# Kernel tuning notes

Hardware: AMD Instinct MI355X
Metric: run time of the kernel (lower is better)

Reference implementation:

```python
import jax, jax.numpy as jnp
import numpy as np

N_NODES = 500000


def _gconv(x, src, dst, ew, w_neigh, b, w_self):
    # DGL GraphConv(norm='none'): multiply weight first (in>=out here), then aggregate.
    h = x @ w_neigh                      # [N, out]
    msg = h[src] * ew[:, None]           # [E, out]
    agg = jax.ops.segment_sum(msg, dst, num_segments=N_NODES)
    return agg + b + x @ w_self          # neigh conv (+bias) + self-loop linear (no bias)


def setup_inputs() -> dict:
    key = jax.random.key(0)
    ks = jax.random.split(key, 16)
    N, E, G, F = N_NODES, 16000000, 64, 16
    inp = {
        "x": jax.random.normal(ks[0], (N, F), jnp.float32),
        "src": jax.random.randint(ks[1], (E,), 0, N),
        "dst": jax.random.randint(ks[2], (E,), 0, N),
        "graph_id": jnp.sort(jax.random.randint(ks[3], (N,), 0, G)),
        "edge_weight": jax.random.uniform(ks[4], (E,), jnp.float32),
        "num_graphs": G,
        "w_neigh0": jax.random.normal(ks[5], (F, 1), jnp.float32),
        "b0": jax.random.normal(ks[6], (1,), jnp.float32),
        "w_self0": jax.random.normal(ks[7], (F, 1), jnp.float32),
        "w_neigh1": jax.random.normal(ks[8], (1, 1), jnp.float32),
        "b1": jax.random.normal(ks[9], (1,), jnp.float32),
        "w_self1": jax.random.normal(ks[10], (1, 1), jnp.float32),
        "w_neigh2": jax.random.normal(ks[11], (1, 1), jnp.float32),
        "b2": jax.random.normal(ks[12], (1,), jnp.float32),
        "w_self2": jax.random.normal(ks[13], (1, 1), jnp.float32),
        "fc1_w": jax.random.normal(ks[14], (8, 1), jnp.float32),
        "fc1_b": jax.random.normal(ks[15], (8,), jnp.float32),
        "out_w": jax.random.normal(jax.random.fold_in(key, 100), (4, 8), jnp.float32),
        "out_b": jax.random.normal(jax.random.fold_in(key, 101), (4,), jnp.float32),
    }
    return inp


def reference(x, src, dst, graph_id, edge_weight, num_graphs,
              w_neigh0, b0, w_self0, w_neigh1, b1, w_self1,
              w_neigh2, b2, w_self2, fc1_w, fc1_b, out_w, out_b):
    h = jax.nn.relu(_gconv(x, src, dst, edge_weight, w_neigh0, b0, w_self0))
    h = jax.nn.relu(_gconv(h, src, dst, edge_weight, w_neigh1, b1, w_self1))
    h = jax.nn.relu(_gconv(h, src, dst, edge_weight, w_neigh2, b2, w_self2))
    # dgl.sum_nodes: per-graph segment sum over batched graph -> [G, 1]
    hg = jax.ops.segment_sum(h, graph_id, num_segments=num_graphs)
    hg2 = jax.nn.sigmoid((hg @ fc1_w.T + fc1_b) * 1000.0)   # [G, 8]
    out = jax.nn.relu(hg2 @ out_w.T + out_b)                # [G, 4]
    return jax.nn.log_softmax(out, axis=1)
```

## Files before the change

### kernel.cpp

```cpp
#include <hip/hip_runtime.h>
#include <hip/hip_fp16.h>

#define N_NODES 500000
#define NGRAPH  64
#define FDIM    16
#define NB1     62
#define NPB1    8192
#define SH1     13
#define SLC     16
#define NBLK    1024
#define CH      4096
typedef unsigned int u32;
typedef unsigned short u16;
typedef unsigned long long u64;

__global__ __launch_bounds__(1024) void proj_hist(const int* __restrict__ dst, int E, int chunk,
                                                  u32* __restrict__ blockHist,
                                                  const float* __restrict__ x,
                                                  const float* __restrict__ wn,
                                                  const float* __restrict__ wsf,
                                                  float* __restrict__ a,
                                                  float* __restrict__ s) {
    __shared__ u32 cnt[NB1];
    if (blockIdx.x < NBLK) {
        if (threadIdx.x < NB1) cnt[threadIdx.x] = 0;
        __syncthreads();
        int b = blockIdx.x;
        int lo = b * chunk, hi = min(lo + chunk, E);
        int m = (hi - lo) & ~3;
        for (int i = lo + threadIdx.x * 4; i < lo + m; i += 4096) {
            int4 d = *(const int4*)(dst + i);
            atomicAdd(&cnt[((u32)d.x) >> SH1], 1u);
            atomicAdd(&cnt[((u32)d.y) >> SH1], 1u);
            atomicAdd(&cnt[((u32)d.z) >> SH1], 1u);
            atomicAdd(&cnt[((u32)d.w) >> SH1], 1u);
        }
        for (int i = lo + m + threadIdx.x; i < hi; i += 1024)
            atomicAdd(&cnt[((u32)dst[i]) >> SH1], 1u);
        __syncthreads();
        if (threadIdx.x < NB1)
            blockHist[(size_t)b * NB1 + threadIdx.x] = cnt[threadIdx.x];
    } else {
        int i = (blockIdx.x - NBLK) * 1024 + threadIdx.x;
        if (i >= N_NODES) return;
        const float4* xr = (const float4*)(x + (size_t)i * FDIM);
        float4 v0 = xr[0], v1 = xr[1], v2 = xr[2], v3 = xr[3];
        const float4* n4 = (const float4*)wn;
        const float4* s4 = (const float4*)wsf;
        float4 n0 = n4[0], n1 = n4[1], n2 = n4[2], n3 = n4[3];
        float4 w0 = s4[0], w1 = s4[1], w2 = s4[2], w3 = s4[3];
        float an = v0.x*n0.x + v0.y*n0.y + v0.z*n0.z + v0.w*n0.w
                 + v1.x*n1.x + v1.y*n1.y + v1.z*n1.z + v1.w*n1.w
                 + v2.x*n2.x + v2.y*n2.y + v2.z*n2.z + v2.w*n2.w
                 + v3.x*n3.x + v3.y*n3.y + v3.z*n3.z + v3.w*n3.w;
        float as = v0.x*w0.x + v0.y*w0.y + v0.z*w0.z + v0.w*w0.w
                 + v1.x*w1.x + v1.y*w1.y + v1.z*w1.z + v1.w*w1.w
                 + v2.x*w2.x + v2.y*w2.y + v2.z*w2.z + v2.w*w2.w
                 + v3.x*w3.x + v3.y*w3.y + v3.z*w3.z + v3.w*w3.w;
        a[i] = an;
        s[i] = as;
    }
}

__global__ __launch_bounds__(NBLK) void scan1_kernel(u32* __restrict__ blockHist,
                                                     u32* __restrict__ binTotal) {
    int j = blockIdx.x;
    __shared__ u32 lsum[NBLK];
    int t = threadIdx.x;
    u32 v = blockHist[(size_t)t * NB1 + j];
    lsum[t] = v;
    __syncthreads();
    u32 x = v;
    for (int off = 1; off < NBLK; off <<= 1) {
        u32 y = (t >= off) ? lsum[t - off] : 0u;
        __syncthreads();
        x += y; lsum[t] = x;
        __syncthreads();
    }
    if (t == NBLK - 1) binTotal[j] = x;
    blockHist[(size_t)t * NB1 + j] = x - v;
}

__global__ void scan2_kernel(const u32* __restrict__ binTotal, u32* __restrict__ binStart) {
    __shared__ u32 sh[64];
    int t = threadIdx.x;
    u32 v = (t < NB1) ? binTotal[t] : 0u;
    sh[t] = v;
    __syncthreads();
    for (int d = 1; d < 64; d <<= 1) {
        u32 y = (t >= d) ? sh[t - d] : 0u;
        __syncthreads();
        sh[t] += y;
        __syncthreads();
    }
    if (t < NB1) binStart[t] = sh[t] - v;
    if (t == 63) binStart[NB1] = sh[63];
}

__global__ __launch_bounds__(512) void scatter_staged(const int* __restrict__ src,
                                                      const int* __restrict__ dst,
                                                      const float* __restrict__ ew,
                                                      int E, int chunk,
                                                      const u32* __restrict__ blockHist,
                                                      const u32* __restrict__ binStart,
                                                      u32* __restrict__ bIdx,
                                                      u16* __restrict__ bW) {
    __shared__ u32 cursor[64];
    __shared__ u32 cnt[64];
    __shared__ u32 off[64];
    __shared__ u64 stage[CH];
    __shared__ unsigned char binOf[CH];
    int b = blockIdx.x, tid = threadIdx.x;
    if (tid < NB1) cursor[tid] = binStart[tid] + blockHist[(size_t)b * NB1 + tid];
    int lo = b * chunk, hiB = min(lo + chunk, E);
    for (int base = lo; base < hiB; base += CH) {
        int n = min(CH, hiB - base);
        if (tid < 64) cnt[tid] = 0;
        __syncthreads();
        u32 rec[8]; u16 wv[8]; u32 bi[8], rk[8];
#pragma unroll
        for (int k = 0; k < 8; ++k) {
            int idx = base + k * 512 + tid;
            bi[k] = 0xFFFFFFFFu;
            if (idx < base + n) {
                u32 d  = (u32)dst[idx];
                bi[k]  = d >> SH1;
                rec[k] = ((u32)src[idx]) | ((d & (NPB1 - 1)) << 19);
                wv[k]  = __half_as_ushort(__float2half(ew[idx]));
                rk[k]  = atomicAdd(&cnt[bi[k]], 1u);
            }
        }
        __syncthreads();
        if (tid < 64) off[tid] = cnt[tid];
        __syncthreads();
        for (int d2 = 1; d2 < 64; d2 <<= 1) {
            u32 y = 0;
            if (tid < 64 && tid >= d2) y = off[tid - d2];
            __syncthreads();
            if (tid < 64) off[tid] += y;
            __syncthreads();
        }
        if (tid < 64) off[tid] -= cnt[tid];
        __syncthreads();
#pragma unroll
        for (int k = 0; k < 8; ++k) {
            if (bi[k] != 0xFFFFFFFFu) {
                u32 p = off[bi[k]] + rk[k];
                stage[p] = (u64)rec[k] | ((u64)wv[k] << 32);
                binOf[p] = (unsigned char)bi[k];
            }
        }
        __syncthreads();
        for (int p = tid; p < n; p += 512) {
            u32 jj = binOf[p];
            u64 e = stage[p];
            u32 gpos = cursor[jj] + ((u32)p - off[jj]);
            bIdx[gpos] = (u32)e;
            bW[gpos]   = (u16)(e >> 32);
        }
        __syncthreads();
        if (tid < NB1) cursor[tid] += cnt[tid];
        __syncthreads();
    }
}

__global__ __launch_bounds__(512) void bin_pass(const u32* __restrict__ bIdx,
                                                const u16* __restrict__ bW,
                                                const u32* __restrict__ binStart,
                                                const float* __restrict__ hsrc,
                                                float* __restrict__ partials) {
    __shared__ float acc[NPB1];
    int j = blockIdx.x / SLC, sl = blockIdx.x % SLC;
    for (int t = threadIdx.x; t < NPB1; t += 512) acc[t] = 0.0f;
    __syncthreads();
    u32 blo = binStart[j], bhi = binStart[j + 1];
    u32 cj = bhi - blo;
    u32 per = (cj + SLC - 1) / SLC;
    u32 lo = blo + sl * per;
    u32 hi = min(lo + per, bhi);
    u32 i = lo + threadIdx.x;
    for (; i + 7u * 512u < hi; i += 8u * 512u) {
        u32 r[8]; u16 w[8];
#pragma unroll
        for (int k = 0; k < 8; ++k) r[k] = __builtin_nontemporal_load(&bIdx[i + (u32)k * 512u]);
#pragma unroll
        for (int k = 0; k < 8; ++k) w[k] = __builtin_nontemporal_load(&bW[i + (u32)k * 512u]);
        float g[8];
#pragma unroll
        for (int k = 0; k < 8; ++k) g[k] = hsrc[r[k] & 0x7FFFFu];
#pragma unroll
        for (int k = 0; k < 8; ++k)
            atomicAdd(&acc[r[k] >> 19], g[k] * __half2float(__ushort_as_half(w[k])));
    }
    for (; i < hi; i += 512) {
        u32 r = __builtin_nontemporal_load(&bIdx[i]);
        u16 w = __builtin_nontemporal_load(&bW[i]);
        atomicAdd(&acc[r >> 19], hsrc[r & 0x7FFFFu] * __half2float(__ushort_as_half(w)));
    }
    __syncthreads();
    float* p = partials + ((size_t)j * SLC + sl) * NPB1;
    for (int t = threadIdx.x; t < NPB1; t += 512)
        __builtin_nontemporal_store(acc[t], &p[t]);
}

template<bool LAST>
__global__ __launch_bounds__(256) void merge_update(const float* __restrict__ partials,
                                                    const float* __restrict__ selfv,
                                                    const float* __restrict__ wnp,
                                                    const float* __restrict__ bp,
                                                    const float* __restrict__ wsp,
                                                    float* __restrict__ hout,
                                                    const int* __restrict__ gid,
                                                    float* __restrict__ hg) {
    int n = blockIdx.x * blockDim.x + threadIdx.x;
    if (n >= N_NODES) return;
    int j = n >> SH1;
    int l = n & (NPB1 - 1);
    const float* p = partials + ((size_t)j * SLC) * NPB1 + l;
    float sum = 0.0f;
#pragma unroll
    for (int k = 0; k < SLC; ++k) sum += __builtin_nontemporal_load(&p[k * NPB1]);
    float scale = wnp ? wnp[0] : 1.0f;
    float wself = wsp ? wsp[0] : 1.0f;
    float v = fmaxf(sum * scale + bp[0] + selfv[n] * wself, 0.0f);
    hout[n] = v;
    if (LAST) {
        int g = gid[n];
        unsigned long long act = __ballot(1);
        int g0 = __shfl(g, 0);
        if (act == ~0ull && __all(g == g0)) {
            float t = v;
#pragma unroll
            for (int o = 32; o > 0; o >>= 1) t += __shfl_down(t, o);
            if ((threadIdx.x & 63) == 0) atomicAdd(&hg[g0], t);
        } else {
            atomicAdd(&hg[g], v);
        }
    }
}

__global__ void edge_pass(const int* __restrict__ src, const int* __restrict__ dst,
                          const float* __restrict__ ew, const float* __restrict__ h,
                          float* __restrict__ agg, const float* __restrict__ wnp, int E) {
    float scale = wnp ? wnp[0] : 1.0f;
    int stride = gridDim.x * blockDim.x;
    for (int i = blockIdx.x * blockDim.x + threadIdx.x; i < E; i += stride)
        atomicAdd(&agg[dst[i]], h[src[i]] * ew[i] * scale);
}
__global__ void node_update(const float* __restrict__ agg, const float* __restrict__ selfv,
                            const float* __restrict__ bp, const float* __restrict__ wsp,
                            float* __restrict__ hout) {
    int i = blockIdx.x * blockDim.x + threadIdx.x;
    if (i >= N_NODES) return;
    float wsc = wsp ? wsp[0] : 1.0f;
    hout[i] = fmaxf(agg[i] + bp[0] + selfv[i] * wsc, 0.0f);
}
__global__ void proj_kernel(const float* __restrict__ x, const float* __restrict__ wn,
                            const float* __restrict__ wsf, float* __restrict__ a,
                            float* __restrict__ s) {
    int i = blockIdx.x * blockDim.x + threadIdx.x;
    if (i >= N_NODES) return;
    float an = 0.f, as = 0.f;
    for (int k = 0; k < FDIM; ++k) {
        float v = x[(size_t)i * FDIM + k];
        an += v * wn[k]; as += v * wsf[k];
    }
    a[i] = an; s[i] = as;
}

__global__ __launch_bounds__(256) void graph_sum(const float* __restrict__ h,
                                                 const int* __restrict__ gid,
                                                 float* __restrict__ hg) {
    __shared__ float loc[NGRAPH];
    int t = threadIdx.x;
    if (t < NGRAPH) loc[t] = 0.0f;
    __syncthreads();
    int nq = N_NODES / 4;
    int stride = gridDim.x * blockDim.x;
    for (int q = blockIdx.x * blockDim.x + t; q < nq; q += stride) {
        int4   g4 = *(const int4*)(gid + 4 * q);
        float4 h4 = *(const float4*)(h + 4 * q);
        int g0 = __shfl(g4.x, 0);
        bool uni = (g4.x == g0) & (g4.w == g0);
        if (__all(uni)) {
            float v = h4.x + h4.y + h4.z + h4.w;
#pragma unroll
            for (int o = 32; o > 0; o >>= 1) v += __shfl_down(v, o);
            if ((t & 63) == 0) atomicAdd(&loc[g0], v);
        } else {
            atomicAdd(&loc[g4.x], h4.x);
            atomicAdd(&loc[g4.y], h4.y);
            atomicAdd(&loc[g4.z], h4.z);
            atomicAdd(&loc[g4.w], h4.w);
        }
    }
    __syncthreads();
    if (t < NGRAPH) atomicAdd(&hg[t], loc[t]);
}

__global__ void head_kernel(const float* __restrict__ hg,
                            const float* __restrict__ fc1w, const float* __restrict__ fc1b,
                            const float* __restrict__ outw, const float* __restrict__ outb,
                            float* __restrict__ out) {
    int g = threadIdx.x;
    if (g >= NGRAPH) return;
    float v = hg[g];
    float t[8];
#pragma unroll
    for (int j = 0; j < 8; ++j) {
        float z = (v * fc1w[j] + fc1b[j]) * 1000.0f;
        t[j] = 1.0f / (1.0f + expf(-z));
    }
    float o[4];
#pragma unroll
    for (int k = 0; k < 4; ++k) {
        float acc2 = outb[k];
#pragma unroll
        for (int j = 0; j < 8; ++j) acc2 += t[j] * outw[k * 8 + j];
        o[k] = fmaxf(acc2, 0.0f);
    }
    float m = fmaxf(fmaxf(o[0], o[1]), fmaxf(o[2], o[3]));
    float se = 0.0f;
#pragma unroll
    for (int k = 0; k < 4; ++k) se += expf(o[k] - m);
    float lse = m + logf(se);
#pragma unroll
    for (int k = 0; k < 4; ++k) out[g * 4 + k] = o[k] - lse;
}

extern "C" void kernel_launch(void* const* d_in, const int* in_sizes, int n_in,
                              void* d_out, int out_size, void* d_ws, size_t ws_size,
                              hipStream_t stream) {
    const float* x    = (const float*)d_in[0];
    const int*   src  = (const int*)  d_in[1];
    const int*   dst  = (const int*)  d_in[2];
    const int*   gid  = (const int*)  d_in[3];
    const float* ew   = (const float*)d_in[4];
    const float* wn0  = (const float*)d_in[6];
    const float* b0   = (const float*)d_in[7];
    const float* ws0  = (const float*)d_in[8];
    const float* wn1  = (const float*)d_in[9];
    const float* b1   = (const float*)d_in[10];
    const float* ws1  = (const float*)d_in[11];
    const float* wn2  = (const float*)d_in[12];
    const float* b2   = (const float*)d_in[13];
    const float* ws2  = (const float*)d_in[14];
    const float* fc1w = (const float*)d_in[15];
    const float* fc1b = (const float*)d_in[16];
    const float* outw = (const float*)d_in[17];
    const float* outb = (const float*)d_in[18];
    int E = in_sizes[1];

    const int BLK = 256;
    int nodeGrid = (N_NODES + BLK - 1) / BLK;
    char* ws = (char*)d_ws;

    size_t off = 0;
    u32* bIdx       = (u32*)(ws + off); off += (size_t)E * 4;
    u16* bW         = (u16*)(ws + off); off += (size_t)E * 2;
    off = (off + 63) & ~(size_t)63;
    u32* blockHist  = (u32*)(ws + off); off += (size_t)NBLK * NB1 * 4;
    u32* binStart   = (u32*)(ws + off); off += (NB1 + 2) * 4;
    off = (off + 63) & ~(size_t)63;
    u32* binTotal   = (u32*)(ws + off); off += (NB1 + 2) * 4;
    off = (off + 63) & ~(size_t)63;
    float* partials = (float*)(ws + off); off += (size_t)NB1 * SLC * NPB1 * 4;
    float* a  = (float*)(ws + off); off += (size_t)N_NODES * 4;
    float* s  = (float*)(ws + off); off += (size_t)N_NODES * 4;
    float* hg = (float*)(ws + off); off += 256;
    size_t need = off;

    if (ws_size >= need) {
        int chunk = (((E + NBLK - 1) / NBLK) + 3) & ~3;
        int projBlocks = (N_NODES + 1023) / 1024;

        proj_hist<<<NBLK + projBlocks, 1024, 0, stream>>>(dst, E, chunk, blockHist,
                                                          x, wn0, ws0, a, s);
        scan1_kernel<<<NB1, NBLK, 0, stream>>>(blockHist, binTotal);
        scan2_kernel<<<1, 64, 0, stream>>>(binTotal, binStart);
        scatter_staged<<<NBLK, 512, 0, stream>>>(src, dst, ew, E, chunk, blockHist,
                                                 binStart, bIdx, bW);
        (void)hipMemsetAsync(hg, 0, NGRAPH * sizeof(float), stream);

        bin_pass<<<NB1 * SLC, 512, 0, stream>>>(bIdx, bW, binStart, a, partials);
        merge_update<false><<<nodeGrid, BLK, 0, stream>>>(partials, s, nullptr, b0, nullptr,
                                                          s, gid, hg);
        bin_pass<<<NB1 * SLC, 512, 0, stream>>>(bIdx, bW, binStart, s, partials);
        merge_update<false><<<nodeGrid, BLK, 0, stream>>>(partials, s, wn1, b1, ws1,
                                                          s, gid, hg);
        bin_pass<<<NB1 * SLC, 512, 0, stream>>>(bIdx, bW, binStart, s, partials);
        merge_update<true><<<nodeGrid, BLK, 0, stream>>>(partials, s, wn2, b2, ws2,
                                                         s, gid, hg);

        head_kernel<<<1, 64, 0, stream>>>(hg, fc1w, fc1b, outw, outb, (float*)d_out);
    } else {
        float* wsb  = (float*)d_ws;
        float* fa   = wsb;
        float* fs   = wsb + 1 * (size_t)N_NODES;
        float* fagg = wsb + 2 * (size_t)N_NODES;
        float* fh   = wsb + 3 * (size_t)N_NODES;
        float* fhg  = wsb + 4 * (size_t)N_NODES;

        proj_kernel<<<nodeGrid, BLK, 0, stream>>>(x, wn0, ws0, fa, fs);

        (void)hipMemsetAsync(fagg, 0, (size_t)N_NODES * sizeof(float), stream);
        edge_pass<<<4096, BLK, 0, stream>>>(src, dst, ew, fa, fagg, nullptr, E);
        node_update<<<nodeGrid, BLK, 0, stream>>>(fagg, fs, b0, nullptr, fh);

        (void)hipMemsetAsync(fagg, 0, (size_t)N_NODES * sizeof(float), stream);
        edge_pass<<<4096, BLK, 0, stream>>>(src, dst, ew, fh, fagg, wn1, E);
        node_update<<<nodeGrid, BLK, 0, stream>>>(fagg, fh, b1, ws1, fh);

        (void)hipMemsetAsync(fagg, 0, (size_t)N_NODES * sizeof(float), stream);
        edge_pass<<<4096, BLK, 0, stream>>>(src, dst, ew, fh, fagg, wn2, E);
        node_update<<<nodeGrid, BLK, 0, stream>>>(fagg, fh, b2, ws2, fh);

        (void)hipMemsetAsync(fhg, 0, NGRAPH * sizeof(float), stream);
        graph_sum<<<512, 256, 0, stream>>>(fh, gid, fhg);
        head_kernel<<<1, 64, 0, stream>>>(fhg, fc1w, fc1b, outw, outb, (float*)d_out);
    }
}
```

Baseline: 480.8 us.

## Pack binned edge index and fp32 weight into one 64-bit record, halve slices

Replaces the split index (u32) and fp16 weight (u16) arrays with a single interleaved u64 array holding the packed index and a full fp32 weight. This gives one coalesced load per edge in the bin pass and keeps the weight at full precision. The cost is that each edge now takes 8 bytes instead of 6, so more bytes are read in each of the three bin passes and written in the scatter. SLC drops from 16 to 8, which halves the partial buffers the merge step must read but also halves the number of bin_pass blocks.

```diff
diff --git a/kernel.cpp b/kernel.cpp
--- a/kernel.cpp
+++ b/kernel.cpp
@@ -1,5 +1,4 @@
 #include <hip/hip_runtime.h>
-#include <hip/hip_fp16.h>
 
 #define N_NODES 500000
 #define NGRAPH  64
@@ -7,11 +6,10 @@
 #define NB1     62
 #define NPB1    8192
 #define SH1     13
-#define SLC     16
+#define SLC     8
 #define NBLK    1024
 #define CH      4096
 typedef unsigned int u32;
-typedef unsigned short u16;
 typedef unsigned long long u64;
 
 __global__ __launch_bounds__(1024) void proj_hist(const int* __restrict__ dst, int E, int chunk,
@@ -103,8 +101,7 @@
                                                       int E, int chunk,
                                                       const u32* __restrict__ blockHist,
                                                       const u32* __restrict__ binStart,
-                                                      u32* __restrict__ bIdx,
-                                                      u16* __restrict__ bW) {
+                                                      u64* __restrict__ binned) {
     __shared__ u32 cursor[64];
     __shared__ u32 cnt[64];
     __shared__ u32 off[64];
@@ -117,7 +114,7 @@
         int n = min(CH, hiB - base);
         if (tid < 64) cnt[tid] = 0;
         __syncthreads();
-        u32 rec[8]; u16 wv[8]; u32 bi[8], rk[8];
+        u32 rec[8]; float wv[8]; u32 bi[8], rk[8];
 #pragma unroll
         for (int k = 0; k < 8; ++k) {
             int idx = base + k * 512 + tid;
@@ -126,7 +123,7 @@
                 u32 d  = (u32)dst[idx];
                 bi[k]  = d >> SH1;
                 rec[k] = ((u32)src[idx]) | ((d & (NPB1 - 1)) << 19);
-                wv[k]  = __half_as_ushort(__float2half(ew[idx]));
+                wv[k]  = ew[idx];
                 rk[k]  = atomicAdd(&cnt[bi[k]], 1u);
             }
         }
@@ -146,17 +143,14 @@
         for (int k = 0; k < 8; ++k) {
             if (bi[k] != 0xFFFFFFFFu) {
                 u32 p = off[bi[k]] + rk[k];
-                stage[p] = (u64)rec[k] | ((u64)wv[k] << 32);
+                stage[p] = (u64)rec[k] | ((u64)__float_as_uint(wv[k]) << 32);
                 binOf[p] = (unsigned char)bi[k];
             }
         }
         __syncthreads();
         for (int p = tid; p < n; p += 512) {
             u32 jj = binOf[p];
-            u64 e = stage[p];
-            u32 gpos = cursor[jj] + ((u32)p - off[jj]);
-            bIdx[gpos] = (u32)e;
-            bW[gpos]   = (u16)(e >> 32);
+            binned[cursor[jj] + ((u32)p - off[jj])] = stage[p];
         }
         __syncthreads();
         if (tid < NB1) cursor[tid] += cnt[tid];
@@ -164,8 +158,7 @@
     }
 }
 
-__global__ __launch_bounds__(512) void bin_pass(const u32* __restrict__ bIdx,
-                                                const u16* __restrict__ bW,
+__global__ __launch_bounds__(512) void bin_pass(const u64* __restrict__ binned,
                                                 const u32* __restrict__ binStart,
                                                 const float* __restrict__ hsrc,
                                                 float* __restrict__ partials) {
@@ -180,22 +173,19 @@
     u32 hi = min(lo + per, bhi);
     u32 i = lo + threadIdx.x;
     for (; i + 7u * 512u < hi; i += 8u * 512u) {
-        u32 r[8]; u16 w[8];
-#pragma unroll
-        for (int k = 0; k < 8; ++k) r[k] = __builtin_nontemporal_load(&bIdx[i + (u32)k * 512u]);
-#pragma unroll
-        for (int k = 0; k < 8; ++k) w[k] = __builtin_nontemporal_load(&bW[i + (u32)k * 512u]);
+        u64 e[8];
+#pragma unroll
+        for (int k = 0; k < 8; ++k) e[k] = __builtin_nontemporal_load(&binned[i + (u32)k * 512u]);
         float g[8];
 #pragma unroll
-        for (int k = 0; k < 8; ++k) g[k] = hsrc[r[k] & 0x7FFFFu];
+        for (int k = 0; k < 8; ++k) g[k] = hsrc[((u32)e[k]) & 0x7FFFFu];
 #pragma unroll
         for (int k = 0; k < 8; ++k)
-            atomicAdd(&acc[r[k] >> 19], g[k] * __half2float(__ushort_as_half(w[k])));
+            atomicAdd(&acc[((u32)e[k]) >> 19], g[k] * __uint_as_float((u32)(e[k] >> 32)));
     }
     for (; i < hi; i += 512) {
-        u32 r = __builtin_nontemporal_load(&bIdx[i]);
-        u16 w = __builtin_nontemporal_load(&bW[i]);
-        atomicAdd(&acc[r >> 19], hsrc[r & 0x7FFFFu] * __half2float(__ushort_as_half(w)));
+        u64 e = __builtin_nontemporal_load(&binned[i]);
+        atomicAdd(&acc[((u32)e) >> 19], hsrc[((u32)e) & 0x7FFFFu] * __uint_as_float((u32)(e >> 32)));
     }
     __syncthreads();
     float* p = partials + ((size_t)j * SLC + sl) * NPB1;
@@ -356,9 +346,7 @@
     char* ws = (char*)d_ws;
 
     size_t off = 0;
-    u32* bIdx       = (u32*)(ws + off); off += (size_t)E * 4;
-    u16* bW         = (u16*)(ws + off); off += (size_t)E * 2;
-    off = (off + 63) & ~(size_t)63;
+    u64* binned     = (u64*)(ws + off); off += (size_t)E * 8;
     u32* blockHist  = (u32*)(ws + off); off += (size_t)NBLK * NB1 * 4;
     u32* binStart   = (u32*)(ws + off); off += (NB1 + 2) * 4;
     off = (off + 63) & ~(size_t)63;
@@ -379,16 +367,16 @@
         scan1_kernel<<<NB1, NBLK, 0, stream>>>(blockHist, binTotal);
         scan2_kernel<<<1, 64, 0, stream>>>(binTotal, binStart);
         scatter_staged<<<NBLK, 512, 0, stream>>>(src, dst, ew, E, chunk, blockHist,
-                                                 binStart, bIdx, bW);
+                                                 binStart, binned);
         (void)hipMemsetAsync(hg, 0, NGRAPH * sizeof(float), stream);
 
-        bin_pass<<<NB1 * SLC, 512, 0, stream>>>(bIdx, bW, binStart, a, partials);
+        bin_pass<<<NB1 * SLC, 512, 0, stream>>>(binned, binStart, a, partials);
         merge_update<false><<<nodeGrid, BLK, 0, stream>>>(partials, s, nullptr, b0, nullptr,
                                                           s, gid, hg);
-        bin_pass<<<NB1 * SLC, 512, 0, stream>>>(bIdx, bW, binStart, s, partials);
+        bin_pass<<<NB1 * SLC, 512, 0, stream>>>(binned, binStart, s, partials);
         merge_update<false><<<nodeGrid, BLK, 0, stream>>>(partials, s, wn1, b1, ws1,
                                                           s, gid, hg);
-        bin_pass<<<NB1 * SLC, 512, 0, stream>>>(bIdx, bW, binStart, s, partials);
+        bin_pass<<<NB1 * SLC, 512, 0, stream>>>(binned, binStart, s, partials);
         merge_update<true><<<nodeGrid, BLK, 0, stream>>>(partials, s, wn2, b2, ws2,
                                                          s, gid, hg);
 
```

New measurement: 467.0 us. -2.9%, faster.
